# Optimization experiments

Measured on AMD Instinct MI355X. Metric: run time of the kernel, lower is better.

The kernel has to match this reference:

```python
import jax, jax.numpy as jnp
import numpy as np

C, H, W = 16, 512, 512
HID = 128
N_STEPS = 8


def setup_inputs() -> dict:
    key = jax.random.key(0)
    k1, k2, k3 = jax.random.split(key, 3)
    state = jax.random.normal(k1, (C, H, W), dtype=jnp.float32)
    # MLP params: 5*C = 80 gathered features -> HID -> C delta channels
    W1 = jax.random.normal(k2, (5 * C, HID), dtype=jnp.float32) * (1.0 / np.sqrt(5 * C))
    b1 = jnp.zeros((HID,), dtype=jnp.float32)
    W2 = jax.random.normal(k3, (HID, C), dtype=jnp.float32) * (1.0 / np.sqrt(HID))
    b2 = jnp.zeros((C,), dtype=jnp.float32)
    return {"state": state, "W1": W1, "b1": b1, "W2": W2, "b2": b2, "n_steps": N_STEPS}


def _neighbor_idx(n):
    i = jnp.arange(n)
    minus = jnp.maximum(i - 1, 0)          # clamp at low edge (cy==0 -> 0)
    plus = jnp.where(i == n - 1, 0, i + 1)  # WRAP to 0 at high edge (original quirk)
    return minus, plus


def reference(state, W1, b1, W2, b2, n_steps):
    c, h, w = state.shape
    up, down = _neighbor_idx(h)
    left, right = _neighbor_idx(w)

    def step(s, _):
        # von-Neumann gather: (5C, H, W), feature order [center, up, down, left, right]
        feats = jnp.concatenate(
            [s, s[:, up, :], s[:, down, :], s[:, :, left], s[:, :, right]], axis=0)
        x = feats.reshape(5 * c, h * w).T        # (HW, 5C)
        hdn = jax.nn.relu(x @ W1 + b1)           # (HW, HID)
        delta = (hdn @ W2 + b2).T.reshape(c, h, w)
        s_new = s + delta
        s_new = s_new.at[0].set(s[0])            # channel 0 snapshot restore
        return s_new, None

    out, _ = jax.lax.scan(step, state, None, length=n_steps)
    return out
```

## Files before the change

kernel.cpp:

```cpp
#include <hip/hip_runtime.h>
#include <hip/hip_bf16.h>

#define HH 512
#define WW 512
#define CC 16
#define HIDN 128
#define HWSZ (HH*WW)

typedef __attribute__((ext_vector_type(8))) short short8;
typedef __attribute__((ext_vector_type(4))) short short4v;
typedef __attribute__((ext_vector_type(4))) float float4v;

__device__ __forceinline__ short to_bf16(float f){
    __hip_bfloat16 h = __float2bfloat16(f);
    return __builtin_bit_cast(short, h);
}

__global__ void __launch_bounds__(256) prep_kernel(
    const float* __restrict__ W1, const float* __restrict__ W2,
    short* __restrict__ w1t, short* __restrict__ w2t)
{
    int t = blockIdx.x * blockDim.x + threadIdx.x;
    int stride = gridDim.x * blockDim.x;
    for (int idx = t; idx < HIDN*96; idx += stride){
        int n = idx / 96;
        int k = idx - n*96;
        float v = (k < 80) ? W1[k*HIDN + n] : 0.0f;
        w1t[idx] = to_bf16(v);
    }
    for (int idx = t; idx < CC*HIDN; idx += stride){
        int n = idx >> 7;
        int k = idx & 127;
        w2t[idx] = to_bf16(W2[k*CC + n]);
    }
}

#define RSTRIDE 24
#define RROW    (68*RSTRIDE)

__global__ void __launch_bounds__(256, 5) step_kernel(
    const float* __restrict__ src, float* __restrict__ dst,
    const short* __restrict__ w1t, const short* __restrict__ w2t,
    const float* __restrict__ b1, const float* __restrict__ b2)
{
    __shared__ __align__(16) short rows_u[3*RROW];
    __shared__ __align__(16) short hdn[64][136];
    __shared__ __align__(16) float sctr[64][16];
    __shared__ float b1s[HIDN];
    __shared__ float b2s[CC];

    float (*stg)[65] = (float (*)[65])rows_u;

    const int t    = threadIdx.x;
    const int w    = t >> 6;
    const int lane = t & 63;
    const int ln15 = lane & 15;
    const int g4   = lane >> 4;

    const int bx = blockIdx.x;
    const int y  = bx >> 3;
    const int xs = (bx & 7) << 6;

    if (t < HIDN) b1s[t] = b1[t];
    if (t < CC)   b2s[t] = b2[t];

    const int yu = (y == 0)      ? 0 : (y - 1);
    const int yd = (y == HH - 1) ? 0 : (y + 1);

    if (t < 192){
        const int r  = t >> 6;
        const int l  = t & 63;
        const int q  = l & 15;
        const int cq = l >> 4;
        const int rowg = (r == 0) ? y : ((r == 1) ? yu : yd);
        const float* base = src + (size_t)rowg * WW + xs + (q << 2);
        float4v f[4];
        #pragma unroll
        for (int i = 0; i < 4; ++i)
            f[i] = *(const float4v*)(base + (size_t)((cq << 2) + i) * HWSZ);
        #pragma unroll
        for (int j = 0; j < 4; ++j){
            short4v v;
            v[0] = to_bf16(f[0][j]); v[1] = to_bf16(f[1][j]);
            v[2] = to_bf16(f[2][j]); v[3] = to_bf16(f[3][j]);
            *(short4v*)&rows_u[r*RROW + ((q << 2) + 1 + j)*RSTRIDE + (cq << 2)] = v;
            if (r == 0){
                float4v g = {f[0][j], f[1][j], f[2][j], f[3][j]};
                *(float4v*)&sctr[(q << 2) + j][cq << 2] = g;
            }
        }
    } else if (t < 224){
        const int c    = (t - 192) & 15;
        const int side = (t - 192) >> 4;
        const int gx   = (side == 0) ? ((xs == 0) ? 0 : xs - 1)
                                     : ((xs + 64 == WW) ? 0 : xs + 64);
        rows_u[(side * 65)*RSTRIDE + c] =
            to_bf16(src[(size_t)c*HWSZ + (size_t)y*WW + gx]);
    }
    __syncthreads();

    int offA[3];
    #pragma unroll
    for (int kk = 0; kk < 3; ++kk){
        const int g  = (kk < 2) ? ((kk << 2) + g4) : (8 + (g4 & 1));
        const int n  = g >> 1;
        const int cb = (g & 1) << 3;
        const int r  = (n == 1) ? 1 : ((n == 2) ? 2 : 0);
        const int dx = (n == 3) ? -1 : ((n == 4) ? 1 : 0);
        offA[kk] = r*RROW + (ln15 + 1 + dx)*RSTRIDE + cb;
    }

    float4v acc[4][2];
    #pragma unroll
    for (int mt = 0; mt < 4; ++mt)
        #pragma unroll
        for (int nt = 0; nt < 2; ++nt)
            acc[mt][nt] = (float4v){0.f, 0.f, 0.f, 0.f};

    #pragma unroll
    for (int kk = 0; kk < 3; ++kk){
        short8 bfrag[2];
        #pragma unroll
        for (int nt = 0; nt < 2; ++nt){
            const int col = (w << 5) + (nt << 4) + ln15;
            bfrag[nt] = *(const short8*)(w1t + col * 96 + (kk << 5) + (g4 << 3));
        }
        #pragma unroll
        for (int mt = 0; mt < 4; ++mt){
            short8 afrag = *(const short8*)(&rows_u[offA[kk] + mt * (16 * RSTRIDE)]);
            #pragma unroll
            for (int nt = 0; nt < 2; ++nt){
                acc[mt][nt] = __builtin_amdgcn_mfma_f32_16x16x32_bf16(
                    afrag, bfrag[nt], acc[mt][nt], 0, 0, 0);
            }
        }
    }

    #pragma unroll
    for (int nt = 0; nt < 2; ++nt){
        const int col  = (w << 5) + (nt << 4) + ln15;
        const float bias = b1s[col];
        #pragma unroll
        for (int mt = 0; mt < 4; ++mt){
            #pragma unroll
            for (int r = 0; r < 4; ++r){
                const int m = (mt << 4) + (g4 << 2) + r;
                float v = acc[mt][nt][r] + bias;
                v = v > 0.f ? v : 0.f;
                hdn[m][col] = to_bf16(v);
            }
        }
    }
    __syncthreads();

    float4v acc2 = (float4v){0.f, 0.f, 0.f, 0.f};
    #pragma unroll
    for (int kk = 0; kk < 4; ++kk){
        const int k0 = kk << 5;
        short8 a = *(const short8*)(&hdn[(w << 4) + ln15][k0 + (g4 << 3)]);
        short8 b = *(const short8*)(w2t + ln15 * HIDN + k0 + (g4 << 3));
        acc2 = __builtin_amdgcn_mfma_f32_16x16x32_bf16(a, b, acc2, 0, 0, 0);
    }

    {
        const int c = ln15;
        const float bias2 = b2s[c];
        #pragma unroll
        for (int r = 0; r < 4; ++r){
            const int p = (w << 4) + (g4 << 2) + r;
            const float sold = sctr[p][c];
            float v = (c == 0) ? sold : (sold + acc2[r] + bias2);
            stg[c][p] = v;
        }
    }
    __syncthreads();

    #pragma unroll
    for (int i = 0; i < 4; ++i){
        const int idx = t + (i << 8);
        const int c2  = idx >> 6;
        const int xo  = idx & 63;
        dst[(size_t)c2 * HWSZ + (size_t)y * WW + xs + xo] = stg[c2][xo];
    }
}

extern "C" void kernel_launch(void* const* d_in, const int* in_sizes, int n_in,
                              void* d_out, int out_size, void* d_ws, size_t ws_size,
                              hipStream_t stream)
{
    const float* state = (const float*)d_in[0];
    const float* W1    = (const float*)d_in[1];
    const float* b1    = (const float*)d_in[2];
    const float* W2    = (const float*)d_in[3];
    const float* b2    = (const float*)d_in[4];

    float* B1  = (float*)d_ws;
    short* w1t = (short*)((char*)d_ws + (size_t)HWSZ * CC * 4);
    short* w2t = w1t + HIDN * 96;
    float* out = (float*)d_out;

    prep_kernel<<<32, 256, 0, stream>>>(W1, W2, w1t, w2t);

    dim3 grid(HH * (WW / 64));
    step_kernel<<<grid, 256, 0, stream>>>(state, B1, w1t, w2t, b1, b2);
    step_kernel<<<grid, 256, 0, stream>>>(B1, out, w1t, w2t, b1, b2);
    step_kernel<<<grid, 256, 0, stream>>>(out, B1, w1t, w2t, b1, b2);
    step_kernel<<<grid, 256, 0, stream>>>(B1, out, w1t, w2t, b1, b2);
    step_kernel<<<grid, 256, 0, stream>>>(out, B1, w1t, w2t, b1, b2);
    step_kernel<<<grid, 256, 0, stream>>>(B1, out, w1t, w2t, b1, b2);
    step_kernel<<<grid, 256, 0, stream>>>(out, B1, w1t, w2t, b1, b2);
    step_kernel<<<grid, 256, 0, stream>>>(B1, out, w1t, w2t, b1, b2);
}
```

Measured before the change: 262.0 us.

## Swap MFMA operand roles in layer 1 and write outputs directly from registers

The first GEMM is transposed so that W1 rows supply the A operand and pixel features supply B. As a result the hidden activations are written to shared memory as packed 4-element vectors instead of scalar stores. The center-state staging in shared memory, the output staging buffer and its extra barrier are removed. Each lane instead re-reads its four old state values from global memory and writes float4 results straight to dst. Biases are read from global memory rather than being copied into shared memory. The aim is to cut LDS traffic, shared-memory footprint and one synchronization, at the cost of an extra global read of the center values.

```diff
diff --git a/kernel.cpp b/kernel.cpp
--- a/kernel.cpp
+++ b/kernel.cpp
@@ -45,11 +45,6 @@
 {
     __shared__ __align__(16) short rows_u[3*RROW];
     __shared__ __align__(16) short hdn[64][136];
-    __shared__ __align__(16) float sctr[64][16];
-    __shared__ float b1s[HIDN];
-    __shared__ float b2s[CC];
-
-    float (*stg)[65] = (float (*)[65])rows_u;
 
     const int t    = threadIdx.x;
     const int w    = t >> 6;
@@ -60,9 +55,6 @@
     const int bx = blockIdx.x;
     const int y  = bx >> 3;
     const int xs = (bx & 7) << 6;
-
-    if (t < HIDN) b1s[t] = b1[t];
-    if (t < CC)   b2s[t] = b2[t];
 
     const int yu = (y == 0)      ? 0 : (y - 1);
     const int yd = (y == HH - 1) ? 0 : (y + 1);
@@ -84,10 +76,6 @@
             v[0] = to_bf16(f[0][j]); v[1] = to_bf16(f[1][j]);
             v[2] = to_bf16(f[2][j]); v[3] = to_bf16(f[3][j]);
             *(short4v*)&rows_u[r*RROW + ((q << 2) + 1 + j)*RSTRIDE + (cq << 2)] = v;
-            if (r == 0){
-                float4v g = {f[0][j], f[1][j], f[2][j], f[3][j]};
-                *(float4v*)&sctr[(q << 2) + j][cq << 2] = g;
-            }
         }
     } else if (t < 224){
         const int c    = (t - 192) & 15;
@@ -97,9 +85,8 @@
         rows_u[(side * 65)*RSTRIDE + c] =
             to_bf16(src[(size_t)c*HWSZ + (size_t)y*WW + gx]);
     }
-    __syncthreads();
 
-    int offA[3];
+    int offB[3];
     #pragma unroll
     for (int kk = 0; kk < 3; ++kk){
         const int g  = (kk < 2) ? ((kk << 2) + g4) : (8 + (g4 & 1));
@@ -107,51 +94,57 @@
         const int cb = (g & 1) << 3;
         const int r  = (n == 1) ? 1 : ((n == 2) ? 2 : 0);
         const int dx = (n == 3) ? -1 : ((n == 4) ? 1 : 0);
-        offA[kk] = r*RROW + (ln15 + 1 + dx)*RSTRIDE + cb;
+        offB[kk] = r*RROW + (ln15 + 1 + dx)*RSTRIDE + cb;
     }
 
-    float4v acc[4][2];
+    __syncthreads();
+
+    float4v acc[2][4];
     #pragma unroll
-    for (int mt = 0; mt < 4; ++mt)
+    for (int mt = 0; mt < 2; ++mt)
         #pragma unroll
-        for (int nt = 0; nt < 2; ++nt)
+        for (int nt = 0; nt < 4; ++nt)
             acc[mt][nt] = (float4v){0.f, 0.f, 0.f, 0.f};
 
     #pragma unroll
     for (int kk = 0; kk < 3; ++kk){
-        short8 bfrag[2];
+        short8 bfragF[4];
         #pragma unroll
-        for (int nt = 0; nt < 2; ++nt){
-            const int col = (w << 5) + (nt << 4) + ln15;
-            bfrag[nt] = *(const short8*)(w1t + col * 96 + (kk << 5) + (g4 << 3));
-        }
+        for (int nt = 0; nt < 4; ++nt)
+            bfragF[nt] = *(const short8*)(&rows_u[offB[kk] + nt * (16 * RSTRIDE)]);
         #pragma unroll
-        for (int mt = 0; mt < 4; ++mt){
-            short8 afrag = *(const short8*)(&rows_u[offA[kk] + mt * (16 * RSTRIDE)]);
+        for (int mt = 0; mt < 2; ++mt){
+            const int hrow = (((w << 1) + mt) << 4) + ln15;
+            short8 afragW = *(const short8*)(w1t + hrow * 96 + (kk << 5) + (g4 << 3));
             #pragma unroll
-            for (int nt = 0; nt < 2; ++nt){
+            for (int nt = 0; nt < 4; ++nt)
                 acc[mt][nt] = __builtin_amdgcn_mfma_f32_16x16x32_bf16(
-                    afrag, bfrag[nt], acc[mt][nt], 0, 0, 0);
-            }
+                    afragW, bfragF[nt], acc[mt][nt], 0, 0, 0);
         }
     }
 
     #pragma unroll
-    for (int nt = 0; nt < 2; ++nt){
-        const int col  = (w << 5) + (nt << 4) + ln15;
-        const float bias = b1s[col];
+    for (int mt = 0; mt < 2; ++mt){
+        const int hbase = (((w << 1) + mt) << 4) + (g4 << 2);
+        const float4v bb = *(const float4v*)(b1 + hbase);
         #pragma unroll
-        for (int mt = 0; mt < 4; ++mt){
+        for (int nt = 0; nt < 4; ++nt){
+            short4v s;
             #pragma unroll
             for (int r = 0; r < 4; ++r){
-                const int m = (mt << 4) + (g4 << 2) + r;
-                float v = acc[mt][nt][r] + bias;
+                float v = acc[mt][nt][r] + bb[r];
                 v = v > 0.f ? v : 0.f;
-                hdn[m][col] = to_bf16(v);
+                s[r] = to_bf16(v);
             }
+            *(short4v*)&hdn[(nt << 4) + ln15][hbase] = s;
         }
     }
     __syncthreads();
+
+    const int pxb = (w << 4) + (g4 << 2);
+    const size_t gofs = (size_t)ln15 * HWSZ + (size_t)y * WW + xs + pxb;
+    const float4v sold = *(const float4v*)(src + gofs);
+    const float bias2 = b2[ln15];
 
     float4v acc2 = (float4v){0.f, 0.f, 0.f, 0.f};
     #pragma unroll
@@ -162,26 +155,13 @@
         acc2 = __builtin_amdgcn_mfma_f32_16x16x32_bf16(a, b, acc2, 0, 0, 0);
     }
 
-    {
-        const int c = ln15;
-        const float bias2 = b2s[c];
-        #pragma unroll
-        for (int r = 0; r < 4; ++r){
-            const int p = (w << 4) + (g4 << 2) + r;
-            const float sold = sctr[p][c];
-            float v = (c == 0) ? sold : (sold + acc2[r] + bias2);
-            stg[c][p] = v;
-        }
+    float4v outv;
+    #pragma unroll
+    for (int r = 0; r < 4; ++r){
+        const float v = sold[r] + acc2[r] + bias2;
+        outv[r] = (ln15 == 0) ? sold[r] : v;
     }
-    __syncthreads();
-
-    #pragma unroll
-    for (int i = 0; i < 4; ++i){
-        const int idx = t + (i << 8);
-        const int c2  = idx >> 6;
-        const int xo  = idx & 63;
-        dst[(size_t)c2 * HWSZ + (size_t)y * WW + xs + xo] = stg[c2][xo];
-    }
+    *(float4v*)(dst + gofs) = outv;
 }
 
 extern "C" void kernel_launch(void* const* d_in, const int* in_sizes, int n_in,
```

Result: no change. 264.2 us (+0.8%).
